# Kernel optimization log

Measured on AMD Instinct MI355X. Metric: run time of the kernel, lower is better.

## Reference

```python
import jax, jax.numpy as jnp
import numpy as np

NEG_SLOPE = 0.01  # torch nn.LeakyReLU default


def _normalize_adj(A):
    """Faithful port of GraphConvolution.adj_normalize for a non-symmetric A.

    torch builds diag_embed(d_s) and does a batched matmul D @ A; that is
    mathematically a row scaling, expressed here as a broadcast multiply.
    """
    B, N, _ = A.shape
    # rows whose (A + A^T) row-sum is nonzero get a self-loop of 1 on the diagonal
    mask = jnp.sum(A + jnp.swapaxes(A, 1, 2), axis=-1) != 0  # [B, N]
    idx = jnp.arange(N)
    diag = A[:, idx, idx]
    A = A.at[:, idx, idx].set(jnp.where(mask, 1.0, diag))
    d = A.sum(-1)  # [B, N] out-degree
    # asymmetric branch: d_s = d^-1 where d != 0 else 0;  D @ A == d_s[:, :, None] * A
    d_inv = jnp.where(d != 0, 1.0 / d, 0.0)
    return d_inv[..., None] * A


def setup_inputs() -> dict:
    key = jax.random.key(0)
    k1, k2, k3 = jax.random.split(key, 3)
    B, N, D_in, D_out = 8, 2048, 128, 128
    x = jax.random.normal(k1, (B, N, D_in), dtype=jnp.float32)
    A = jax.random.uniform(k2, (B, N, N), dtype=jnp.float32)
    W = jax.random.normal(k3, (D_out, D_in), dtype=jnp.float32) * 0.05
    return {"x": x, "A": A, "W": W}


def reference(x, A, W):
    # adj_normalize(...).detach()
    An = jax.lax.stop_gradient(_normalize_adj(A))  # [B, N, N]
    # fc (no bias) + LeakyReLU
    h = jax.nn.leaky_relu(jnp.einsum('bnd,ed->bne', x, W), negative_slope=NEG_SLOPE)
    # dense aggregation A @ h; dropout(p=0) is identity (eval mode)
    return jnp.einsum('bnm,bme->bne', An, h)
```

## Files before the change

kernel.cpp:

```cpp
#include <hip/hip_runtime.h>
#include <hip/hip_bf16.h>

#define BB 8
#define NN 2048
#define DD 128

typedef float f32x4_t __attribute__((ext_vector_type(4)));
typedef short s16x8_t __attribute__((ext_vector_type(8)));

__device__ __forceinline__ unsigned short f2bf(float f){
  union { float f; unsigned int u; } v; v.f = f;
  unsigned int u = v.u;
  u += 0x7FFFu + ((u >> 16) & 1u);
  return (unsigned short)(u >> 16);
}
__device__ __forceinline__ float bf2f(unsigned short s){
  union { unsigned int u; float f; } v; v.u = ((unsigned int)s) << 16;
  return v.f;
}
__device__ __forceinline__ s16x8_t pack_bf16_8(const float4 lo, const float4 hi){
  union { __hip_bfloat162 p[4]; s16x8_t v; } U;
  U.p[0] = __float22bfloat162_rn(float2{lo.x, lo.y});
  U.p[1] = __float22bfloat162_rn(float2{lo.z, lo.w});
  U.p[2] = __float22bfloat162_rn(float2{hi.x, hi.y});
  U.p[3] = __float22bfloat162_rn(float2{hi.z, hi.w});
  return U.v;
}

__global__ __launch_bounds__(256) void gc_phase1(const float* __restrict__ x,
                                                 const float* __restrict__ W,
                                                 unsigned short* __restrict__ h,
                                                 unsigned short* __restrict__ hT){
  __shared__ float smem[64*132 + 128*128];
  float* xs = smem;
  float* WT = smem + 64*132;

  const int t   = threadIdx.x;
  const int bid = blockIdx.x;
  const int b   = bid & 7;
  const int m0  = (bid >> 3) * 64;

  {
    const int e = t >> 1, d0 = (t & 1) * 64;
    const float* wr = W + e*DD + d0;
    #pragma unroll
    for (int i = 0; i < 64; i += 4){
      float4 wv = *(const float4*)(wr + i);
      WT[(d0+i+0)*128 + e] = wv.x;
      WT[(d0+i+1)*128 + e] = wv.y;
      WT[(d0+i+2)*128 + e] = wv.z;
      WT[(d0+i+3)*128 + e] = wv.w;
    }
  }
  #pragma unroll
  for (int i = 0; i < 8; i++){
    int s = t + i*256;
    int row = s >> 5, c4 = (s & 31) * 4;
    float4 xv = *(const float4*)(x + ((size_t)(b*NN + m0 + row))*DD + c4);
    *(float4*)(xs + row*132 + c4) = xv;
  }
  __syncthreads();

  const int rg = t >> 4, cg = t & 15;
  const int r0 = rg*4, c0 = cg*8;
  float acc[4][8];
  #pragma unroll
  for (int i=0;i<4;i++)
    #pragma unroll
    for (int j=0;j<8;j++) acc[i][j] = 0.f;

  #pragma unroll 2
  for (int d = 0; d < 128; d += 4){
    float4 xv[4];
    #pragma unroll
    for (int i=0;i<4;i++) xv[i] = *(const float4*)(xs + (r0+i)*132 + d);
    #pragma unroll
    for (int dd=0; dd<4; dd++){
      float4 wa = *(const float4*)(WT + (d+dd)*128 + c0);
      float4 wb = *(const float4*)(WT + (d+dd)*128 + c0 + 4);
      #pragma unroll
      for (int i=0;i<4;i++){
        float xq = (dd==0)?xv[i].x:(dd==1)?xv[i].y:(dd==2)?xv[i].z:xv[i].w;
        acc[i][0] += xq*wa.x; acc[i][1] += xq*wa.y;
        acc[i][2] += xq*wa.z; acc[i][3] += xq*wa.w;
        acc[i][4] += xq*wb.x; acc[i][5] += xq*wb.y;
        acc[i][6] += xq*wb.z; acc[i][7] += xq*wb.w;
      }
    }
  }

  unsigned short hb[4][8];
  #pragma unroll
  for (int i=0;i<4;i++){
    s16x8_t st;
    #pragma unroll
    for (int j=0;j<8;j++){
      float v = acc[i][j];
      v = v > 0.f ? v : 0.01f*v;
      hb[i][j] = f2bf(v);
      st[j] = (short)hb[i][j];
    }
    *(s16x8_t*)(h + ((size_t)(b*NN + m0 + r0 + i))*DD + c0) = st;
  }

  __syncthreads();
  unsigned short* Tb = (unsigned short*)smem;
  #pragma unroll
  for (int i=0;i<4;i++)
    #pragma unroll
    for (int j=0;j<8;j++)
      Tb[(c0+j)*72 + (r0+i)] = hb[i][j];
  __syncthreads();

  {
    const int e = t >> 1, mh = (t & 1) * 32;
    unsigned short* dst = hT + ((size_t)(b*DD + e))*NN + m0 + mh;
    #pragma unroll
    for (int i = 0; i < 32; i += 8)
      *(s16x8_t*)(dst + i) = *(const s16x8_t*)(Tb + e*72 + mh + i);
  }
}

__global__ __launch_bounds__(256, 2) void gc_main(const float* __restrict__ A,
                                                  const unsigned short* __restrict__ h,
                                                  const unsigned short* __restrict__ hT,
                                                  float* __restrict__ out){
  __shared__ float red[2][16*128];
  __shared__ float rsred[2][16];

  const int tid = threadIdx.x;
  const int w = tid >> 6, l = tid & 63;
  const int bid = blockIdx.x;
  const int b  = bid & 7;
  const int xt = bid >> 3;
  const int wpair = w & 1;
  const int khalf = w >> 1;
  const int wm0 = xt*32 + wpair*16;
  const int rl = l & 15, kc = l >> 4;
  const int myrow = wm0 + rl;
  const int k0 = khalf * 1024;

  const float* Arow = A + ((size_t)(b*NN + myrow))*NN + k0 + kc*8;
  const unsigned short* hTb = hT + (size_t)b * DD * NN;

  const float diagv = (khalf == 0) ? A[((size_t)(b*NN + myrow))*NN + myrow] : 0.f;

  const unsigned short* Bp[8];
  #pragma unroll
  for (int n=0;n<8;n++) Bp[n] = hTb + (size_t)(n*16 + rl)*NN + k0 + kc*8;

  f32x4_t acc[8];
  #pragma unroll
  for (int n=0;n<8;n++) acc[n] = (f32x4_t){0.f,0.f,0.f,0.f};
  float rsum = 0.f;

  s16x8_t Bcur[8], Bnxt[8];
  float4 a0,a1, b0,b1, c0,c1;

  #pragma unroll
  for (int n=0;n<8;n++) Bcur[n] = *(const s16x8_t*)(Bp[n]);
  { const float* ap = Arow;      a0 = *(const float4*)ap; a1 = *(const float4*)(ap+4); }
  { const float* ap = Arow + 32; b0 = *(const float4*)ap; b1 = *(const float4*)(ap+4); }

  #pragma unroll 4
  for (int s = 0; s < 32; s++){
    const int sn = (s+1 < 32) ? s+1 : 31;
    const int sp = (s+2 < 32) ? s+2 : 31;
    #pragma unroll
    for (int n=0;n<8;n++) Bnxt[n] = *(const s16x8_t*)(Bp[n] + sn*32);
    { const float* ap = Arow + sp*32; c0 = *(const float4*)ap; c1 = *(const float4*)(ap+4); }

    rsum += (a0.x+a0.y)+(a0.z+a0.w) + (a1.x+a1.y)+(a1.z+a1.w);
    s16x8_t af = pack_bf16_8(a0,a1);
    #pragma unroll
    for (int n=0;n<8;n++)
      acc[n] = __builtin_amdgcn_mfma_f32_16x16x32_bf16(af, Bcur[n], acc[n], 0,0,0);

    a0=b0; a1=b1; b0=c0; b1=c1;
    #pragma unroll
    for (int n=0;n<8;n++) Bcur[n] = Bnxt[n];
  }

  rsum += __shfl_xor(rsum, 16);
  rsum += __shfl_xor(rsum, 32);

  if (khalf == 1){
    float* rb_ = &red[wpair][0];
    #pragma unroll
    for (int n=0;n<8;n++)
      #pragma unroll
      for (int j=0;j<4;j++)
        rb_[(kc*4+j)*128 + n*16 + rl] = acc[n][j];
    if (l < 16) rsred[wpair][l] = rsum;
  }
  __syncthreads();
  if (khalf == 0){
    const float rall = rsum + rsred[wpair][rl];
    const float dinv = 1.0f / (rall - diagv + 1.0f);
    const float dfac = 1.0f - bf2f(f2bf(diagv));
    const float* rb_ = &red[wpair][0];
    const unsigned short* hb_ = h + (size_t)b * NN * DD;
    float* outb = out + (size_t)b * NN * DD;
    #pragma unroll
    for (int j = 0; j < 4; j++){
      const int row_l = kc*4 + j;
      const int rowg = wm0 + row_l;
      const float dj = __shfl(dinv, row_l);
      const float fj = __shfl(dfac, row_l);
      #pragma unroll
      for (int n = 0; n < 8; n++){
        const int col = n*16 + rl;
        const float part = acc[n][j] + rb_[row_l*128 + col];
        const float hv = bf2f(hb_[(size_t)rowg*DD + col]);
        outb[(size_t)rowg*DD + col] = dj * (part + fj * hv);
      }
    }
  }
}

extern "C" void kernel_launch(void* const* d_in, const int* in_sizes, int n_in,
                              void* d_out, int out_size, void* d_ws, size_t ws_size,
                              hipStream_t stream){
  const float* x = (const float*)d_in[0];
  const float* A = (const float*)d_in[1];
  const float* W = (const float*)d_in[2];
  float* out = (float*)d_out;

  unsigned short* h  = (unsigned short*)d_ws;
  unsigned short* hT = h + (size_t)BB*NN*DD;

  gc_phase1<<<dim3(256), dim3(256), 0, stream>>>(x, W, h, hT);
  gc_main  <<<dim3(512), dim3(256), 0, stream>>>(A, h, hT, out);
}
```

Measured before the change: 265.1 us.

## Tile main GEMM through swizzled LDS with async B staging and split-K reduce kernel

The aggregation kernel now stages 64-row A tiles (converted to bf16) and hT tiles into XOR-swizzled, double-buffered shared memory. hT goes through global_load_lds, so each block reuses B across 64 rows instead of every wave loading it straight from global. The K split across the two halves now runs in separate blocks, which write fp32 partial products and row sums to workspace. A new reduce kernel combines them and applies the normalization and self-loop correction. This trades extra workspace traffic and a third launch for better B reuse and coalesced A loads.

```diff
diff --git a/kernel.cpp b/kernel.cpp
--- a/kernel.cpp
+++ b/kernel.cpp
@@ -7,6 +7,7 @@
 
 typedef float f32x4_t __attribute__((ext_vector_type(4)));
 typedef short s16x8_t __attribute__((ext_vector_type(8)));
+typedef short s16x4_t __attribute__((ext_vector_type(4)));
 
 __device__ __forceinline__ unsigned short f2bf(float f){
   union { float f; unsigned int u; } v; v.f = f;
@@ -17,14 +18,6 @@
 __device__ __forceinline__ float bf2f(unsigned short s){
   union { unsigned int u; float f; } v; v.u = ((unsigned int)s) << 16;
   return v.f;
-}
-__device__ __forceinline__ s16x8_t pack_bf16_8(const float4 lo, const float4 hi){
-  union { __hip_bfloat162 p[4]; s16x8_t v; } U;
-  U.p[0] = __float22bfloat162_rn(float2{lo.x, lo.y});
-  U.p[1] = __float22bfloat162_rn(float2{lo.z, lo.w});
-  U.p[2] = __float22bfloat162_rn(float2{hi.x, hi.y});
-  U.p[3] = __float22bfloat162_rn(float2{hi.z, hi.w});
-  return U.v;
 }
 
 __global__ __launch_bounds__(256) void gc_phase1(const float* __restrict__ x,
@@ -122,100 +115,151 @@
 }
 
 __global__ __launch_bounds__(256, 2) void gc_main(const float* __restrict__ A,
-                                                  const unsigned short* __restrict__ h,
                                                   const unsigned short* __restrict__ hT,
-                                                  float* __restrict__ out){
-  __shared__ float red[2][16*128];
-  __shared__ float rsred[2][16];
+                                                  float* __restrict__ Cpart,
+                                                  float* __restrict__ RSpart){
+  __shared__ unsigned short Asw[2][64*64];
+  __shared__ unsigned short Bsw[2][128*64];
 
   const int tid = threadIdx.x;
   const int w = tid >> 6, l = tid & 63;
   const int bid = blockIdx.x;
-  const int b  = bid & 7;
-  const int xt = bid >> 3;
-  const int wpair = w & 1;
-  const int khalf = w >> 1;
-  const int wm0 = xt*32 + wpair*16;
+  const int b    = bid & 7;
+  const int rest = bid >> 3;
+  const int kh   = rest & 1;
+  const int m0   = (rest >> 1) * 64;
+  const int k0   = kh * 1024;
+
   const int rl = l & 15, kc = l >> 4;
-  const int myrow = wm0 + rl;
-  const int k0 = khalf * 1024;
-
-  const float* Arow = A + ((size_t)(b*NN + myrow))*NN + k0 + kc*8;
-  const unsigned short* hTb = hT + (size_t)b * DD * NN;
-
-  const float diagv = (khalf == 0) ? A[((size_t)(b*NN + myrow))*NN + myrow] : 0.f;
-
-  const unsigned short* Bp[8];
-  #pragma unroll
-  for (int n=0;n<8;n++) Bp[n] = hTb + (size_t)(n*16 + rl)*NN + k0 + kc*8;
+
+  const float* Ab = A + (size_t)b*NN*NN;
+  const unsigned short* hTb = hT + (size_t)b*DD*NN;
+
+  const int e_base = w*32 + (l>>3);
+  const int csw    = (l&7) ^ ((l>>3)&7);
+  const unsigned short* bsrc0 = hTb + (size_t)e_base*NN + k0 + csw*8;
+
+  auto stageB = [&](int bi, int t){
+    #pragma unroll
+    for (int q = 0; q < 4; q++){
+      const unsigned short* src = bsrc0 + (size_t)q*8*NN + t*64;
+      unsigned short* dst = &Bsw[bi][(w*32 + q*8)*64];
+      __builtin_amdgcn_global_load_lds((const __attribute__((address_space(1))) void*)src,
+                                       (__attribute__((address_space(3))) void*)dst,
+                                       16, 0, 0);
+    }
+  };
+
+  const int ar_ = tid >> 4;
+  const int ac_ = tid & 15;
+  const float* asrc0 = Ab + (size_t)(m0 + ar_)*NN + k0 + ac_*4;
+
+  float4 av[4];
+  auto loadA = [&](int t){
+    #pragma unroll
+    for (int i = 0; i < 4; i++)
+      av[i] = *(const float4*)(asrc0 + (size_t)(16*i)*NN + t*64);
+  };
+
+  float rs[4] = {0.f,0.f,0.f,0.f};
+  const int cw = ac_ >> 1, sub = ac_ & 1;
+  auto writeA = [&](int bi){
+    #pragma unroll
+    for (int i = 0; i < 4; i++){
+      rs[i] += (av[i].x+av[i].y)+(av[i].z+av[i].w);
+      const int r = ar_ + 16*i;
+      union { __hip_bfloat162 p[2]; s16x4_t v; } U;
+      U.p[0] = __float22bfloat162_rn(float2{av[i].x, av[i].y});
+      U.p[1] = __float22bfloat162_rn(float2{av[i].z, av[i].w});
+      *(s16x4_t*)&Asw[bi][r*64 + ((cw ^ (r&7))<<3) + sub*4] = U.v;
+    }
+  };
 
   f32x4_t acc[8];
   #pragma unroll
   for (int n=0;n<8;n++) acc[n] = (f32x4_t){0.f,0.f,0.f,0.f};
-  float rsum = 0.f;
-
-  s16x8_t Bcur[8], Bnxt[8];
-  float4 a0,a1, b0,b1, c0,c1;
-
-  #pragma unroll
-  for (int n=0;n<8;n++) Bcur[n] = *(const s16x8_t*)(Bp[n]);
-  { const float* ap = Arow;      a0 = *(const float4*)ap; a1 = *(const float4*)(ap+4); }
-  { const float* ap = Arow + 32; b0 = *(const float4*)ap; b1 = *(const float4*)(ap+4); }
-
-  #pragma unroll 4
-  for (int s = 0; s < 32; s++){
-    const int sn = (s+1 < 32) ? s+1 : 31;
-    const int sp = (s+2 < 32) ? s+2 : 31;
-    #pragma unroll
-    for (int n=0;n<8;n++) Bnxt[n] = *(const s16x8_t*)(Bp[n] + sn*32);
-    { const float* ap = Arow + sp*32; c0 = *(const float4*)ap; c1 = *(const float4*)(ap+4); }
-
-    rsum += (a0.x+a0.y)+(a0.z+a0.w) + (a1.x+a1.y)+(a1.z+a1.w);
-    s16x8_t af = pack_bf16_8(a0,a1);
-    #pragma unroll
-    for (int n=0;n<8;n++)
-      acc[n] = __builtin_amdgcn_mfma_f32_16x16x32_bf16(af, Bcur[n], acc[n], 0,0,0);
-
-    a0=b0; a1=b1; b0=c0; b1=c1;
-    #pragma unroll
-    for (int n=0;n<8;n++) Bcur[n] = Bnxt[n];
-  }
-
-  rsum += __shfl_xor(rsum, 16);
-  rsum += __shfl_xor(rsum, 32);
-
-  if (khalf == 1){
-    float* rb_ = &red[wpair][0];
-    #pragma unroll
-    for (int n=0;n<8;n++)
-      #pragma unroll
-      for (int j=0;j<4;j++)
-        rb_[(kc*4+j)*128 + n*16 + rl] = acc[n][j];
-    if (l < 16) rsred[wpair][l] = rsum;
-  }
-  __syncthreads();
-  if (khalf == 0){
-    const float rall = rsum + rsred[wpair][rl];
-    const float dinv = 1.0f / (rall - diagv + 1.0f);
-    const float dfac = 1.0f - bf2f(f2bf(diagv));
-    const float* rb_ = &red[wpair][0];
-    const unsigned short* hb_ = h + (size_t)b * NN * DD;
-    float* outb = out + (size_t)b * NN * DD;
-    #pragma unroll
-    for (int j = 0; j < 4; j++){
-      const int row_l = kc*4 + j;
-      const int rowg = wm0 + row_l;
-      const float dj = __shfl(dinv, row_l);
-      const float fj = __shfl(dfac, row_l);
+
+  stageB(0, 0);
+  loadA(0);
+  writeA(0);
+  __syncthreads();
+
+  const int arow = w*16 + rl;
+  for (int t = 0; t < 16; t++){
+    const int cur = t & 1, nx = cur ^ 1;
+    if (t < 15){ stageB(nx, t+1); loadA(t+1); }
+    #pragma unroll
+    for (int kk = 0; kk < 2; kk++){
+      const s16x8_t afrag = *(const s16x8_t*)&Asw[cur][arow*64 + (((kk*4+kc) ^ (rl&7))<<3)];
       #pragma unroll
       for (int n = 0; n < 8; n++){
-        const int col = n*16 + rl;
-        const float part = acc[n][j] + rb_[row_l*128 + col];
-        const float hv = bf2f(hb_[(size_t)rowg*DD + col]);
-        outb[(size_t)rowg*DD + col] = dj * (part + fj * hv);
+        const int e = n*16 + rl;
+        const s16x8_t bfrag = *(const s16x8_t*)&Bsw[cur][e*64 + (((kk*4+kc) ^ (rl&7))<<3)];
+        acc[n] = __builtin_amdgcn_mfma_f32_16x16x32_bf16(afrag, bfrag, acc[n], 0,0,0);
       }
     }
-  }
+    if (t < 15) writeA(nx);
+    __syncthreads();
+  }
+
+  #pragma unroll
+  for (int i=0;i<4;i++){
+    rs[i] += __shfl_xor(rs[i], 1);
+    rs[i] += __shfl_xor(rs[i], 2);
+    rs[i] += __shfl_xor(rs[i], 4);
+    rs[i] += __shfl_xor(rs[i], 8);
+  }
+  if ((l & 15) == 0){
+    #pragma unroll
+    for (int i=0;i<4;i++)
+      RSpart[((size_t)kh*BB + b)*NN + m0 + ar_ + 16*i] = rs[i];
+  }
+
+  float* Cp = Cpart + (((size_t)kh*BB + b)*NN + m0)*DD;
+  #pragma unroll
+  for (int j = 0; j < 4; j++){
+    const int row_l = w*16 + kc*4 + j;
+    #pragma unroll
+    for (int n = 0; n < 8; n++)
+      Cp[(size_t)row_l*DD + n*16 + rl] = acc[n][j];
+  }
+}
+
+__global__ __launch_bounds__(256) void gc_reduce(const float* __restrict__ A,
+                                                 const unsigned short* __restrict__ h,
+                                                 const float* __restrict__ Cpart,
+                                                 const float* __restrict__ RSpart,
+                                                 float* __restrict__ out){
+  const int tid = threadIdx.x;
+  const int bid = blockIdx.x;
+  const int b   = bid & 7;
+  const int row = (bid >> 3)*16 + (tid >> 4);
+  const int e0  = (tid & 15) * 8;
+
+  const float rsum = RSpart[(size_t)b*NN + row] + RSpart[((size_t)BB + b)*NN + row];
+  const float diag = A[((size_t)b*NN + row)*NN + row];
+  const float dinv = 1.0f / (rsum - diag + 1.0f);
+  const float dfac = 1.0f - bf2f(f2bf(diag));
+
+  const size_t off = ((size_t)b*NN + row)*DD + e0;
+  const float* c0 = Cpart + ((size_t)b*NN + row)*DD + e0;
+  const float* c1 = Cpart + (((size_t)BB + b)*NN + row)*DD + e0;
+  float4 p0a = *(const float4*)(c0),   p0b = *(const float4*)(c0+4);
+  float4 p1a = *(const float4*)(c1),   p1b = *(const float4*)(c1+4);
+  s16x8_t hv = *(const s16x8_t*)(h + off);
+
+  float4 oa, ob;
+  oa.x = dinv*(p0a.x + p1a.x + dfac*bf2f((unsigned short)hv[0]));
+  oa.y = dinv*(p0a.y + p1a.y + dfac*bf2f((unsigned short)hv[1]));
+  oa.z = dinv*(p0a.z + p1a.z + dfac*bf2f((unsigned short)hv[2]));
+  oa.w = dinv*(p0a.w + p1a.w + dfac*bf2f((unsigned short)hv[3]));
+  ob.x = dinv*(p0b.x + p1b.x + dfac*bf2f((unsigned short)hv[4]));
+  ob.y = dinv*(p0b.y + p1b.y + dfac*bf2f((unsigned short)hv[5]));
+  ob.z = dinv*(p0b.z + p1b.z + dfac*bf2f((unsigned short)hv[6]));
+  ob.w = dinv*(p0b.w + p1b.w + dfac*bf2f((unsigned short)hv[7]));
+
+  *(float4*)(out + off)     = oa;
+  *(float4*)(out + off + 4) = ob;
 }
 
 extern "C" void kernel_launch(void* const* d_in, const int* in_sizes, int n_in,
@@ -228,7 +272,10 @@
 
   unsigned short* h  = (unsigned short*)d_ws;
   unsigned short* hT = h + (size_t)BB*NN*DD;
-
-  gc_phase1<<<dim3(256), dim3(256), 0, stream>>>(x, W, h, hT);
-  gc_main  <<<dim3(512), dim3(256), 0, stream>>>(A, h, hT, out);
-}
+  float* Cpart  = (float*)((char*)d_ws + (size_t)16*1024*1024);
+  float* RSpart = (float*)((char*)d_ws + (size_t)33*1024*1024);
+
+  gc_phase1<<<dim3(256),  dim3(256), 0, stream>>>(x, W, h, hT);
+  gc_main  <<<dim3(512),  dim3(256), 0, stream>>>(A, hT, Cpart, RSpart);
+  gc_reduce<<<dim3(1024), dim3(256), 0, stream>>>(A, h, Cpart, RSpart, out);
+}
```

Result: faster. 229.0 us (-13.6%).
